# Performance work log

Hardware: AMD Instinct MI355X
Metric: run time of the kernel (lower is better)

Reference implementation:

```python
import jax, jax.numpy as jnp
import numpy as np

B, S, D, H = 2, 2048, 2048, 16
HD = D // H
THETA = 10000.0


def _rope(t, pos):
    # t: [B, H, S, hd], pos: [S] int -> rotary position embedding (half-split form)
    half = t.shape[-1] // 2
    inv_freq = 1.0 / (THETA ** (jnp.arange(half, dtype=jnp.float32) / half))
    ang = pos[:, None].astype(jnp.float32) * inv_freq[None, :]  # [S, half]
    cos, sin = jnp.cos(ang), jnp.sin(ang)
    t1, t2 = t[..., :half], t[..., half:]
    return jnp.concatenate([t1 * cos - t2 * sin, t1 * sin + t2 * cos], axis=-1)


def setup_inputs() -> dict:
    key = jax.random.key(0)
    ks = jax.random.split(key, 5)
    scale = 1.0 / np.sqrt(D)
    return {
        "x": jax.random.normal(ks[0], (B, S, D), dtype=jnp.float32),
        "Wq": jax.random.normal(ks[1], (D, D), dtype=jnp.float32) * scale,
        "Wk": jax.random.normal(ks[2], (D, D), dtype=jnp.float32) * scale,
        "Wv": jax.random.normal(ks[3], (D, D), dtype=jnp.float32) * scale,
        "Wo": jax.random.normal(ks[4], (D, D), dtype=jnp.float32) * scale,
        "token_positions": jnp.arange(S, dtype=jnp.int32),
    }


def reference(x, Wq, Wk, Wv, Wo, token_positions):
    b, s, d = x.shape
    # fused QKV projection (nn.Linear: y = x @ W.T)
    q = (x @ Wq.T).reshape(b, s, H, HD).transpose(0, 2, 1, 3)  # [B,H,S,hd]
    k = (x @ Wk.T).reshape(b, s, H, HD).transpose(0, 2, 1, 3)
    v = (x @ Wv.T).reshape(b, s, H, HD).transpose(0, 2, 1, 3)
    q = _rope(q, token_positions)
    k = _rope(k, token_positions)
    scale = 1.0 / np.sqrt(HD)
    scores = jnp.einsum("bhqd,bhkd->bhqk", q, k) * scale  # [B,H,S,S]
    causal = jnp.triu(jnp.ones((s, s), dtype=bool), k=1)
    scores = jnp.where(causal, jnp.float32(-jnp.inf), scores)
    attn = jax.nn.softmax(scores, axis=-1)
    o = jnp.einsum("bhqk,bhkd->bhqd", attn, v)  # [B,H,S,hd]
    o = o.transpose(0, 2, 1, 3).reshape(b, s, d)
    return o @ Wo.T
```

## Files before the change

kernel.cpp:

```cpp
#include <hip/hip_runtime.h>
#include <math.h>

#define B_  2
#define S_  2048
#define D_  2048
#define H_  16
#define HD_ 128

using u16 = unsigned short;
using u32 = unsigned int;
typedef __attribute__((ext_vector_type(4))) float f32x4;
typedef __attribute__((ext_vector_type(8))) short bf16x8;
using u16x4_t = __attribute__((ext_vector_type(4))) unsigned short;
using u16x8_t = __attribute__((ext_vector_type(8))) unsigned short;
typedef __attribute__((ext_vector_type(2))) u32 u32x2;
typedef __attribute__((ext_vector_type(4))) u32 u32x4;

__device__ __forceinline__ u16 f2bf(float f) {
  u32 u = __builtin_bit_cast(u32, f);
  u32 r = u + 0x7fffu + ((u >> 16) & 1u);
  return (u16)(r >> 16);
}
__device__ __forceinline__ float bf2f(u16 x) {
  u32 u = ((u32)x) << 16;
  return __builtin_bit_cast(float, u);
}
__device__ __forceinline__ void async_copy16(const u16* g, u16* l) {
  __builtin_amdgcn_global_load_lds((const __attribute__((address_space(1))) u32*)g,
                                   (__attribute__((address_space(3))) u32*)l, 16, 0, 0);
}

__global__ void cvt_f32_bf16(const float* __restrict__ src, u16* __restrict__ dst, int n) {
  int i = (blockIdx.x * blockDim.x + threadIdx.x) * 4;
  if (i >= n) return;
  float4 v = *(const float4*)(src + i);
  u16x4_t o;
  o[0] = f2bf(v.x); o[1] = f2bf(v.y); o[2] = f2bf(v.z); o[3] = f2bf(v.w);
  *(u16x4_t*)(dst + i) = o;
}

__global__ void rope_table(const int* __restrict__ pos, float2* __restrict__ tab) {
  int t = blockIdx.x * blockDim.x + threadIdx.x;
  if (t >= S_ * 64) return;
  int s = t >> 6, i = t & 63;
  float freq = expf(-(float)i * (9.210340371976184f / 64.0f));
  float ang = (float)pos[s] * freq;
  tab[t] = make_float2(cosf(ang), sinf(ang));
}

__global__ void rope_apply(u16* __restrict__ Q, u16* __restrict__ K,
                           const float2* __restrict__ tab) {
  int t = blockIdx.x * blockDim.x + threadIdx.x;
  int g = t & 15;
  int bsh = t >> 4;
  int h = bsh & (H_ - 1);
  int bs = bsh >> 4;
  int s = bs & (S_ - 1);
  size_t base = (size_t)bs * D_ + (size_t)h * HD_;
  int d2 = g * 4;
  const float2* tb = &tab[s * 64 + d2];
  float2 cs[4];
  #pragma unroll
  for (int j = 0; j < 4; ++j) cs[j] = tb[j];
  #pragma unroll
  for (int which = 0; which < 2; ++which) {
    u16* P = which ? K : Q;
    u16x4_t a = *(u16x4_t*)(P + base + d2);
    u16x4_t c = *(u16x4_t*)(P + base + 64 + d2);
    u16x4_t ra, rc;
    #pragma unroll
    for (int j = 0; j < 4; ++j) {
      float t1 = bf2f(a[j]), t2 = bf2f(c[j]);
      ra[j] = f2bf(t1 * cs[j].x - t2 * cs[j].y);
      rc[j] = f2bf(t1 * cs[j].y + t2 * cs[j].x);
    }
    *(u16x4_t*)(P + base + d2) = ra;
    *(u16x4_t*)(P + base + 64 + d2) = rc;
  }
}

template <bool F32OUT>
__global__ void gemm_bt(const u16* __restrict__ A, const u16* __restrict__ Bt,
                        void* __restrict__ Cout, int M, int N, int K) {
  __shared__ u16 lA[128 * 32];
  __shared__ u16 lB[128 * 32];
  const int tid = threadIdx.x;
  const int lane = tid & 63;
  const int w = tid >> 6;
  const int wr = w >> 1, wc = w & 1;
  const int bm = blockIdx.x * 128;
  const int bn = blockIdx.y * 128;
  const int fr = lane & 15, fq = lane >> 4;
  f32x4 acc[4][4] = {};
  for (int k0 = 0; k0 < K; k0 += 32) {
    #pragma unroll
    for (int c = w; c < 8; c += 4) {
      const int e = c * 512 + lane * 8;
      const int r = e >> 5, col = e & 31;
      async_copy16(A + (size_t)(bm + r) * K + k0 + col, lA + c * 512);
      async_copy16(Bt + (size_t)(bn + r) * K + k0 + col, lB + c * 512);
    }
    __syncthreads();
    bf16x8 af[4], bfr[4];
    #pragma unroll
    for (int i = 0; i < 4; ++i) {
      af[i]  = *(const bf16x8*)&lA[(wr * 64 + i * 16 + fr) * 32 + fq * 8];
      bfr[i] = *(const bf16x8*)&lB[(wc * 64 + i * 16 + fr) * 32 + fq * 8];
    }
    #pragma unroll
    for (int i = 0; i < 4; ++i)
      #pragma unroll
      for (int j = 0; j < 4; ++j)
        acc[i][j] = __builtin_amdgcn_mfma_f32_16x16x32_bf16(af[i], bfr[j], acc[i][j], 0, 0, 0);
    __syncthreads();
  }
  #pragma unroll
  for (int i = 0; i < 4; ++i)
    #pragma unroll
    for (int j = 0; j < 4; ++j) {
      const int row = bm + wr * 64 + i * 16 + fq * 4;
      const int col = bn + wc * 64 + j * 16 + fr;
      #pragma unroll
      for (int r = 0; r < 4; ++r) {
        const float v = acc[i][j][r];
        if (F32OUT) ((float*)Cout)[(size_t)(row + r) * N + col] = v;
        else        ((u16*)Cout)[(size_t)(row + r) * N + col] = f2bf(v);
      }
    }
}

__global__ void gemm_qkv3(const u16* __restrict__ A, const u16* __restrict__ Bt,
                          u16* __restrict__ Qo, u16* __restrict__ Ko, u16* __restrict__ Vo) {
  __shared__ u16 lA[128 * 32];
  __shared__ u16 lB[128 * 32];
  const int tid = threadIdx.x;
  const int lane = tid & 63;
  const int w = tid >> 6;
  const int wr = w >> 1, wc = w & 1;
  const int bm = blockIdx.x * 128;
  const int bn = blockIdx.y * 128;
  const int fr = lane & 15, fq = lane >> 4;
  const int K = D_;
  f32x4 acc[4][4] = {};
  for (int k0 = 0; k0 < K; k0 += 32) {
    #pragma unroll
    for (int c = w; c < 8; c += 4) {
      const int e = c * 512 + lane * 8;
      const int r = e >> 5, col = e & 31;
      async_copy16(A + (size_t)(bm + r) * K + k0 + col, lA + c * 512);
      async_copy16(Bt + (size_t)(bn + r) * K + k0 + col, lB + c * 512);
    }
    __syncthreads();
    bf16x8 af[4], bfr[4];
    #pragma unroll
    for (int i = 0; i < 4; ++i) {
      af[i]  = *(const bf16x8*)&lA[(wr * 64 + i * 16 + fr) * 32 + fq * 8];
      bfr[i] = *(const bf16x8*)&lB[(wc * 64 + i * 16 + fr) * 32 + fq * 8];
    }
    #pragma unroll
    for (int i = 0; i < 4; ++i)
      #pragma unroll
      for (int j = 0; j < 4; ++j)
        acc[i][j] = __builtin_amdgcn_mfma_f32_16x16x32_bf16(af[i], bfr[j], acc[i][j], 0, 0, 0);
    __syncthreads();
  }
  u16* out = (bn < 2048) ? Qo : (bn < 4096) ? Ko : Vo;
  const int bnl = bn & 2047;
  #pragma unroll
  for (int i = 0; i < 4; ++i)
    #pragma unroll
    for (int j = 0; j < 4; ++j) {
      const int row = bm + wr * 64 + i * 16 + fq * 4;
      const int col = bnl + wc * 64 + j * 16 + fr;
      #pragma unroll
      for (int r = 0; r < 4; ++r)
        out[(size_t)(row + r) * D_ + col] = f2bf(acc[i][j][r]);
    }
}

#define QB 64
#define KB 32
#define PLD 36

__global__ __launch_bounds__(256, 2)
void attn_fwd(const u16* __restrict__ Qg, const u16* __restrict__ Kg,
              const u16* __restrict__ Vg, u16* __restrict__ po0,
              u16* __restrict__ po1, float2* __restrict__ ml) {
  __shared__ u16 lK[2][KB * HD_];
  __shared__ u16 lV[2][HD_ * 40];
  __shared__ u16 lP[4][16 * PLD];
  const int tid = threadIdx.x;
  const int lane = tid & 63;
  const int w = tid >> 6;
  const int fr = lane & 15, fq = lane >> 4;
  const int bh = blockIdx.y;
  const int split = blockIdx.z;
  const size_t base = (size_t)(bh >> 4) * S_ * D_ + (size_t)(bh & 15) * HD_;
  const int xA = blockIdx.x;
  const int qA = xA * QB, qB = (31 - xA) * QB;
  const int ntA = (qA + QB) / KB;
  const int ntB = (qB + QB) / KB;
  const int c = (ntA <= 16) ? (33 - ntA) : 16;
  const int t0 = split ? c : 0;
  const int t1 = split ? ntB : c;
  const float kscale = 0.08838834764831843f * 1.4426950408889634f;

  bf16x8 qfA[4], qfB[4];
  {
    const u16* qpa = Qg + base + (size_t)(qA + w * 16 + fr) * D_ + fq * 8;
    const u16* qpb = Qg + base + (size_t)(qB + w * 16 + fr) * D_ + fq * 8;
    #pragma unroll
    for (int kk = 0; kk < 4; ++kk) {
      qfA[kk] = *(const bf16x8*)(qpa + kk * 32);
      qfB[kk] = *(const bf16x8*)(qpb + kk * 32);
    }
  }
  f32x4 oA[8] = {}, oB[8] = {};
  float mAs = -INFINITY, lAs = 0.f, mBs = -INFINITY, lBs = 0.f;

  auto stageK = [&](int buf, int kv0) {
    #pragma unroll
    for (int cc = w; cc < 8; cc += 4) {
      const int row = cc * 4 + (lane >> 4);
      const int slot = (lane & 15) ^ (row & 7);
      async_copy16(Kg + base + (size_t)(kv0 + row) * D_ + slot * 8, &lK[buf][cc * 512]);
    }
  };
  const int srow = tid >> 3, sc0 = (tid & 7) * 16;
  const u32 swz = (u32)((sc0 >> 4) & 7) << 4;
  const u32 rb = (u32)srow * 2;
  u16x8_t rv0, rv1;
  auto loadV = [&](int kv0) {
    const u16* gv = Vg + base + (size_t)(kv0 + srow) * D_ + sc0;
    rv0 = *(const u16x8_t*)gv; rv1 = *(const u16x8_t*)(gv + 8);
  };
  auto writeV = [&](int buf) {
    char* lv = (char*)&lV[buf][0];
    #pragma unroll
    for (int j = 0; j < 8; ++j) {
      *(u16*)(lv + ((((u32)(sc0 + j) * 80) + rb) ^ swz))     = rv0[j];
      *(u16*)(lv + ((((u32)(sc0 + 8 + j) * 80) + rb) ^ swz)) = rv1[j];
    }
  };

  auto softmax_sw = [&](const f32x4& s0, const f32x4& s1, float& mrow, float& lrow,
                        f32x4* o, int q0t, int kv0) {
    const int qg = q0t + w * 16 + fr;
    const bool notfull = (kv0 + KB - 1 > q0t);
    float v[8];
    #pragma unroll
    for (int r = 0; r < 4; ++r) {
      v[r]     = s0[r] * kscale;
      v[4 + r] = s1[r] * kscale;
      if (notfull) {
        if (kv0 + fq * 4 + r > qg)      v[r]     = -INFINITY;
        if (kv0 + 16 + fq * 4 + r > qg) v[4 + r] = -INFINITY;
      }
    }
    float mx = fmaxf(fmaxf(fmaxf(v[0], v[1]), fmaxf(v[2], v[3])),
                     fmaxf(fmaxf(v[4], v[5]), fmaxf(v[6], v[7])));
    mx = fmaxf(mx, __shfl_xor(mx, 16));
    mx = fmaxf(mx, __shfl_xor(mx, 32));
    const float mn = fmaxf(mrow, mx);
    const float al = exp2f(mrow - mn);
    mrow = mn;
    float p[8];
    #pragma unroll
    for (int j = 0; j < 8; ++j) p[j] = exp2f(v[j] - mn);
    float rs = ((p[0] + p[1]) + (p[2] + p[3])) + ((p[4] + p[5]) + (p[6] + p[7]));
    rs += __shfl_xor(rs, 16);
    rs += __shfl_xor(rs, 32);
    lrow = lrow * al + rs;
    #pragma unroll
    for (int r = 0; r < 4; ++r) {
      lP[w][fr * PLD + fq * 4 + r]      = f2bf(p[r]);
      lP[w][fr * PLD + 16 + fq * 4 + r] = f2bf(p[4 + r]);
    }
    #pragma unroll
    for (int r = 0; r < 4; ++r) {
      const float ab = __shfl(al, fq * 4 + r);
      #pragma unroll
      for (int nb = 0; nb < 8; ++nb) o[nb][r] *= ab;
    }
  };

  auto pv = [&](f32x4* o, const bf16x8* vf) {
    u32x2 pa0 = *(const u32x2*)&lP[w][fr * PLD + fq * 8];
    u32x2 pa1 = *(const u32x2*)&lP[w][fr * PLD + fq * 8 + 4];
    u32x4 pc; pc[0] = pa0[0]; pc[1] = pa0[1]; pc[2] = pa1[0]; pc[3] = pa1[1];
    const bf16x8 pa = __builtin_bit_cast(bf16x8, pc);
    #pragma unroll
    for (int nb = 0; nb < 8; ++nb)
      o[nb] = __builtin_amdgcn_mfma_f32_16x16x32_bf16(pa, vf[nb], o[nb], 0, 0, 0);
  };

  stageK(0, t0 * KB);
  loadV(t0 * KB);
  writeV(0);

  for (int t = t0; t < t1; ++t) {
    const int kv0 = t * KB;
    const int cur = (t - t0) & 1, nxt = cur ^ 1;
    __syncthreads();
    if (t + 1 < t1) {
      stageK(nxt, kv0 + KB);
      loadV(kv0 + KB);
    }

    const bool doA = (t < ntA);
    f32x4 sA0 = {}, sA1 = {}, sB0 = {}, sB1 = {};
    #pragma unroll
    for (int kk = 0; kk < 4; ++kk) {
      const int sl = ((kk * 4 + fq) ^ (fr & 7)) * 16;
      bf16x8 k0f = *(const bf16x8*)((const char*)&lK[cur][0] + fr * 256 + sl);
      bf16x8 k1f = *(const bf16x8*)((const char*)&lK[cur][0] + (16 + fr) * 256 + sl);
      if (doA) {
        sA0 = __builtin_amdgcn_mfma_f32_16x16x32_bf16(k0f, qfA[kk], sA0, 0, 0, 0);
        sA1 = __builtin_amdgcn_mfma_f32_16x16x32_bf16(k1f, qfA[kk], sA1, 0, 0, 0);
      }
      sB0 = __builtin_amdgcn_mfma_f32_16x16x32_bf16(k0f, qfB[kk], sB0, 0, 0, 0);
      sB1 = __builtin_amdgcn_mfma_f32_16x16x32_bf16(k1f, qfB[kk], sB1, 0, 0, 0);
    }

    bf16x8 vf[8];
    #pragma unroll
    for (int nb = 0; nb < 8; ++nb) {
      const u32 off = (((u32)(nb * 16 + fr) * 80) + (u32)fq * 16) ^ ((u32)nb << 4);
      vf[nb] = *(const bf16x8*)((const char*)&lV[cur][0] + off);
    }

    if (doA) { softmax_sw(sA0, sA1, mAs, lAs, oA, qA, kv0); pv(oA, vf); }
    softmax_sw(sB0, sB1, mBs, lBs, oB, qB, kv0);
    pv(oB, vf);

    if (t + 1 < t1) writeV(nxt);
  }

  u16* po = split ? po1 : po0;
  float2* mlp = ml + (size_t)split * (B_ * H_ * S_) + (size_t)bh * S_;
  if (lane < 16) {
    mlp[qA + w * 16 + fr] = make_float2(mAs, lAs);
    mlp[qB + w * 16 + fr] = make_float2(mBs, lBs);
  }
  #pragma unroll
  for (int r = 0; r < 4; ++r) {
    const int rowA = qA + w * 16 + fq * 4 + r;
    const int rowB = qB + w * 16 + fq * 4 + r;
    u16* orA = po + base + (size_t)rowA * D_;
    u16* orB = po + base + (size_t)rowB * D_;
    #pragma unroll
    for (int nb = 0; nb < 8; ++nb) {
      orA[nb * 16 + fr] = f2bf(oA[nb][r]);
      orB[nb * 16 + fr] = f2bf(oB[nb][r]);
    }
  }
}

__global__ void attn_combine(const u16* __restrict__ po0, const u16* __restrict__ po1,
                             const float2* __restrict__ ml, u16* __restrict__ Og) {
  const int idx = blockIdx.x * blockDim.x + threadIdx.x;
  const int d8 = (idx & 15) * 8;
  const int row = idx >> 4;
  const int bh = row >> 11, s = row & (S_ - 1);
  const float2 v0 = ml[row];
  const float2 v1 = ml[B_ * H_ * S_ + row];
  const float m = fmaxf(v0.x, v1.x);
  const float e0 = exp2f(v0.x - m), e1 = exp2f(v1.x - m);
  const float inv = 1.0f / (v0.y * e0 + v1.y * e1);
  const size_t off = (size_t)(bh >> 4) * S_ * D_ + (size_t)s * D_ + (bh & 15) * HD_ + d8;
  u16x8_t a = *(const u16x8_t*)(po0 + off);
  u16x8_t b = *(const u16x8_t*)(po1 + off);
  u16x8_t o;
  #pragma unroll
  for (int j = 0; j < 8; ++j)
    o[j] = f2bf((bf2f(a[j]) * e0 + bf2f(b[j]) * e1) * inv);
  *(u16x8_t*)(Og + off) = o;
}

extern "C" void kernel_launch(void* const* d_in, const int* in_sizes, int n_in,
                              void* d_out, int out_size, void* d_ws, size_t ws_size,
                              hipStream_t stream) {
  const float* x  = (const float*)d_in[0];
  const float* Wq = (const float*)d_in[1];
  const float* Wk = (const float*)d_in[2];
  const float* Wv = (const float*)d_in[3];
  const float* Wo = (const float*)d_in[4];
  const int* pos  = (const int*)d_in[5];

  char* p = (char*)d_ws;
  u16* xb  = (u16*)p; p += (size_t)B_ * S_ * D_ * 2;
  u16* Wqb = (u16*)p; p += (size_t)D_ * D_ * 2;
  u16* Wkb = (u16*)p; p += (size_t)D_ * D_ * 2;
  u16* Wvb = (u16*)p; p += (size_t)D_ * D_ * 2;
  u16* Wob = (u16*)p; p += (size_t)D_ * D_ * 2;
  u16* Qb  = (u16*)p; p += (size_t)B_ * S_ * D_ * 2;
  u16* Kb  = (u16*)p; p += (size_t)B_ * S_ * D_ * 2;
  u16* Vb  = (u16*)p; p += (size_t)B_ * S_ * D_ * 2;
  float2* tab = (float2*)p; p += (size_t)S_ * 64 * sizeof(float2);
  float2* ml  = (float2*)p; p += (size_t)2 * B_ * H_ * S_ * sizeof(float2);
  u16* po0 = xb;
  u16* po1 = Wqb;
  u16* Ob  = Qb;

  const int nx = B_ * S_ * D_;
  const int nw = D_ * D_;
  cvt_f32_bf16<<<nx / 1024, 256, 0, stream>>>(x,  xb,  nx);
  cvt_f32_bf16<<<nw / 1024, 256, 0, stream>>>(Wq, Wqb, nw);
  cvt_f32_bf16<<<nw / 1024, 256, 0, stream>>>(Wk, Wkb, nw);
  cvt_f32_bf16<<<nw / 1024, 256, 0, stream>>>(Wv, Wvb, nw);
  cvt_f32_bf16<<<nw / 1024, 256, 0, stream>>>(Wo, Wob, nw);
  rope_table<<<(S_ * 64) / 256, 256, 0, stream>>>(pos, tab);

  gemm_qkv3<<<dim3(B_ * S_ / 128, 48), 256, 0, stream>>>(xb, Wqb, Qb, Kb, Vb);

  rope_apply<<<(B_ * S_ * H_ * 16) / 256, 256, 0, stream>>>(Qb, Kb, tab);

  attn_fwd<<<dim3(16, B_ * H_, 2), 256, 0, stream>>>(Qb, Kb, Vb, po0, po1, ml);
  attn_combine<<<(B_ * H_ * S_ * 16) / 256, 256, 0, stream>>>(po0, po1, ml, Ob);

  gemm_bt<true><<<dim3(B_ * S_ / 128, D_ / 128), 256, 0, stream>>>(Ob, Wob, (float*)d_out, B_ * S_, D_, D_);
}
```

Before: 339.7 us.

## Triple-buffer GEMM LDS tiles with async prefetch and XOR-swizzled layout

```diff
diff --git a/kernel.cpp b/kernel.cpp
--- a/kernel.cpp
+++ b/kernel.cpp
@@ -82,8 +82,8 @@
 template <bool F32OUT>
 __global__ void gemm_bt(const u16* __restrict__ A, const u16* __restrict__ Bt,
                         void* __restrict__ Cout, int M, int N, int K) {
-  __shared__ u16 lA[128 * 32];
-  __shared__ u16 lB[128 * 32];
+  __shared__ u16 lA[3][128 * 32];
+  __shared__ u16 lB[3][128 * 32];
   const int tid = threadIdx.x;
   const int lane = tid & 63;
   const int w = tid >> 6;
@@ -91,28 +91,51 @@
   const int bm = blockIdx.x * 128;
   const int bn = blockIdx.y * 128;
   const int fr = lane & 15, fq = lane >> 4;
+  const int KT = K >> 5;
   f32x4 acc[4][4] = {};
-  for (int k0 = 0; k0 < K; k0 += 32) {
+
+  auto stage = [&](int buf, int kt) {
+    const int k0 = kt << 5;
     #pragma unroll
     for (int c = w; c < 8; c += 4) {
-      const int e = c * 512 + lane * 8;
-      const int r = e >> 5, col = e & 31;
-      async_copy16(A + (size_t)(bm + r) * K + k0 + col, lA + c * 512);
-      async_copy16(Bt + (size_t)(bn + r) * K + k0 + col, lB + c * 512);
-    }
-    __syncthreads();
+      const int r = c * 16 + (lane >> 2);
+      const int col = ((lane & 3) ^ ((r >> 1) & 3)) * 8;
+      async_copy16(A + (size_t)(bm + r) * K + k0 + col, &lA[buf][c * 512]);
+      async_copy16(Bt + (size_t)(bn + r) * K + k0 + col, &lB[buf][c * 512]);
+    }
+  };
+
+  stage(0, 0);
+  stage(1, 1);
+  asm volatile("s_waitcnt vmcnt(4)" ::: "memory");
+  __builtin_amdgcn_s_barrier();
+  asm volatile("" ::: "memory");
+
+  int p = 0, sb = 2;
+  #pragma unroll 1
+  for (int kt = 0; kt < KT; ++kt) {
+    if (kt + 2 < KT) stage(sb, kt + 2);
     bf16x8 af[4], bfr[4];
     #pragma unroll
     for (int i = 0; i < 4; ++i) {
-      af[i]  = *(const bf16x8*)&lA[(wr * 64 + i * 16 + fr) * 32 + fq * 8];
-      bfr[i] = *(const bf16x8*)&lB[(wc * 64 + i * 16 + fr) * 32 + fq * 8];
+      const int ra = wr * 64 + i * 16 + fr;
+      const int rb = wc * 64 + i * 16 + fr;
+      af[i]  = *(const bf16x8*)&lA[p][ra * 32 + ((fq ^ ((ra >> 1) & 3)) * 8)];
+      bfr[i] = *(const bf16x8*)&lB[p][rb * 32 + ((fq ^ ((rb >> 1) & 3)) * 8)];
     }
     #pragma unroll
     for (int i = 0; i < 4; ++i)
       #pragma unroll
       for (int j = 0; j < 4; ++j)
         acc[i][j] = __builtin_amdgcn_mfma_f32_16x16x32_bf16(af[i], bfr[j], acc[i][j], 0, 0, 0);
-    __syncthreads();
+    if (kt + 1 < KT) {
+      if (kt + 2 < KT) asm volatile("s_waitcnt vmcnt(4)" ::: "memory");
+      else             asm volatile("s_waitcnt vmcnt(0)" ::: "memory");
+      __builtin_amdgcn_s_barrier();
+      asm volatile("" ::: "memory");
+    }
+    p  = (p == 2) ? 0 : p + 1;
+    sb = (sb == 2) ? 0 : sb + 1;
   }
   #pragma unroll
   for (int i = 0; i < 4; ++i)
@@ -131,8 +154,8 @@
 
 __global__ void gemm_qkv3(const u16* __restrict__ A, const u16* __restrict__ Bt,
                           u16* __restrict__ Qo, u16* __restrict__ Ko, u16* __restrict__ Vo) {
-  __shared__ u16 lA[128 * 32];
-  __shared__ u16 lB[128 * 32];
+  __shared__ u16 lA[3][128 * 32];
+  __shared__ u16 lB[3][128 * 32];
   const int tid = threadIdx.x;
   const int lane = tid & 63;
   const int w = tid >> 6;
@@ -141,28 +164,51 @@
   const int bn = blockIdx.y * 128;
   const int fr = lane & 15, fq = lane >> 4;
   const int K = D_;
+  const int KT = K >> 5;
   f32x4 acc[4][4] = {};
-  for (int k0 = 0; k0 < K; k0 += 32) {
+
+  auto stage = [&](int buf, int kt) {
+    const int k0 = kt << 5;
     #pragma unroll
     for (int c = w; c < 8; c += 4) {
-      const int e = c * 512 + lane * 8;
-      const int r = e >> 5, col = e & 31;
-      async_copy16(A + (size_t)(bm + r) * K + k0 + col, lA + c * 512);
-      async_copy16(Bt + (size_t)(bn + r) * K + k0 + col, lB + c * 512);
-    }
-    __syncthreads();
+      const int r = c * 16 + (lane >> 2);
+      const int col = ((lane & 3) ^ ((r >> 1) & 3)) * 8;
+      async_copy16(A + (size_t)(bm + r) * K + k0 + col, &lA[buf][c * 512]);
+      async_copy16(Bt + (size_t)(bn + r) * K + k0 + col, &lB[buf][c * 512]);
+    }
+  };
+
+  stage(0, 0);
+  stage(1, 1);
+  asm volatile("s_waitcnt vmcnt(4)" ::: "memory");
+  __builtin_amdgcn_s_barrier();
+  asm volatile("" ::: "memory");
+
+  int p = 0, sb = 2;
+  #pragma unroll 1
+  for (int kt = 0; kt < KT; ++kt) {
+    if (kt + 2 < KT) stage(sb, kt + 2);
     bf16x8 af[4], bfr[4];
     #pragma unroll
     for (int i = 0; i < 4; ++i) {
-      af[i]  = *(const bf16x8*)&lA[(wr * 64 + i * 16 + fr) * 32 + fq * 8];
-      bfr[i] = *(const bf16x8*)&lB[(wc * 64 + i * 16 + fr) * 32 + fq * 8];
+      const int ra = wr * 64 + i * 16 + fr;
+      const int rb = wc * 64 + i * 16 + fr;
+      af[i]  = *(const bf16x8*)&lA[p][ra * 32 + ((fq ^ ((ra >> 1) & 3)) * 8)];
+      bfr[i] = *(const bf16x8*)&lB[p][rb * 32 + ((fq ^ ((rb >> 1) & 3)) * 8)];
     }
     #pragma unroll
     for (int i = 0; i < 4; ++i)
       #pragma unroll
       for (int j = 0; j < 4; ++j)
         acc[i][j] = __builtin_amdgcn_mfma_f32_16x16x32_bf16(af[i], bfr[j], acc[i][j], 0, 0, 0);
-    __syncthreads();
+    if (kt + 1 < KT) {
+      if (kt + 2 < KT) asm volatile("s_waitcnt vmcnt(4)" ::: "memory");
+      else             asm volatile("s_waitcnt vmcnt(0)" ::: "memory");
+      __builtin_amdgcn_s_barrier();
+      asm volatile("" ::: "memory");
+    }
+    p  = (p == 2) ? 0 : p + 1;
+    sb = (sb == 2) ? 0 : sb + 1;
   }
   u16* out = (bn < 2048) ? Qo : (bn < 4096) ? Ko : Vo;
   const int bnl = bn & 2047;
```

Result: faster. 328.0 us (-3.4%).
